# Kernel optimization log

Hardware: AMD Instinct MI355X
Metric: run time of the kernel (lower is better)

Reference implementation:

```python
import jax, jax.numpy as jnp
import numpy as np
import math

D, S, B = 64, 2048, 16  # head_dim, seq_len, batch (inputs stored as [D, S, B])


def setup_inputs() -> dict:
    key = jax.random.key(0)
    kq, kk, kv = jax.random.split(key, 3)
    return {
        "Q": jax.random.normal(kq, (D, S, B), dtype=jnp.float32),
        "K": jax.random.normal(kk, (D, S, B), dtype=jnp.float32),
        "V": jax.random.normal(kv, (D, S, B), dtype=jnp.float32),
        "d_k": S,
    }


def reference(Q, K, V, d_k):
    # transpose(0, 2): [D, S, B] -> [B, S, D]
    q = jnp.transpose(Q, (2, 1, 0))
    k = jnp.transpose(K, (2, 1, 0))
    v = jnp.transpose(V, (2, 1, 0))
    # bmm(_Q, K_T) * 1/sqrt(d_k): [B, S, S]
    scores = jnp.einsum("bsd,btd->bst", q, k) * (1.0 / math.sqrt(d_k))
    # original does view(-1, d_k) + Softmax over dim=1; with d_k == last dim
    # this is a softmax over the key axis. Dropout is identity in eval mode.
    probs = jax.nn.softmax(scores, axis=-1)
    out = jnp.einsum("bst,btd->bsd", probs, v)  # [B, S, D]
    # transpose(0, 2) back: [D, S, B]
    return jnp.transpose(out, (2, 1, 0))
```

## Files before the change

kernel.cpp:

```cpp
#include <hip/hip_runtime.h>

#define D_ 64
#define S_ 2048
#define B_ 16
#define QT 64
#define KVT 128

typedef short short8 __attribute__((ext_vector_type(8)));
typedef short short4a __attribute__((ext_vector_type(4)));
typedef float floatx4 __attribute__((ext_vector_type(4)));
typedef unsigned uint2v __attribute__((ext_vector_type(2)));

#define SC2 (1.4426950408889634f / 45.254833995939045f)

__device__ __forceinline__ unsigned short f2bf(float f) {
  unsigned u = __builtin_bit_cast(unsigned, f);
  u += 0x7fffu + ((u >> 16) & 1u);
  return (unsigned short)(u >> 16);
}

__device__ __forceinline__ floatx4 mfma16(short4a a, short4a b, floatx4 c) {
#if __has_builtin(__builtin_amdgcn_mfma_f32_16x16x16bf16_1k)
  return __builtin_amdgcn_mfma_f32_16x16x16bf16_1k(a, b, c, 0, 0, 0);
#else
  floatx4 d;
  asm volatile("v_mfma_f32_16x16x16_bf16 %0, %1, %2, %3"
               : "=v"(d) : "v"(a), "v"(b), "v"(c));
  return d;
#endif
}

__global__ __launch_bounds__(256) void pack_all(const float* __restrict__ Q,
                                                const float* __restrict__ K,
                                                const float* __restrict__ V,
                                                unsigned short* __restrict__ Qp,
                                                unsigned short* __restrict__ Kp,
                                                unsigned short* __restrict__ Vt) {
  __shared__ __align__(16) unsigned short tile[256][72];
  const int t = threadIdx.x;
  const int bid = blockIdx.x;
  if (bid < 256) {
    const bool isK = bid >= 128;
    const float* src = isK ? K : Q;
    unsigned short* dst = isK ? Kp : Qp;
    const float scale = isK ? SC2 : 1.0f;
    const int rb = bid & 127;
    const int s0 = rb * 16;
#pragma unroll
    for (int i = 0; i < 16; i++) {
      int j = i * 256 + t;
      int d = j >> 6;
      int sb4 = (j & 63) * 4;
      const float4 v = *(const float4*)(src + (size_t)d * (S_ * B_) + s0 * B_ + sb4);
      float vv[4] = {v.x, v.y, v.z, v.w};
#pragma unroll
      for (int k = 0; k < 4; k++) {
        int sb = sb4 + k;
        tile[(sb & 15) * 16 + (sb >> 4)][d] = f2bf(vv[k] * scale);
      }
    }
    __syncthreads();
#pragma unroll
    for (int i = 0; i < 8; i++) {
      int j = i * 256 + t;
      int r = j >> 3, c = j & 7;
      int b = r >> 4, si = r & 15;
      uint4 v = *(const uint4*)(&tile[r][c * 8]);
      *(uint4*)(dst + (((size_t)(b * 128 + rb)) << 10) + ((c >> 2) << 9) +
                (((c & 3) * 16 + si) << 3)) = v;
    }
  } else {
    const int vb = bid - 256;
    const int s0 = (vb & 31) * 64;
    const int d0 = (vb >> 5) * 16;
    const int dblk = vb >> 5;
#pragma unroll
    for (int i = 0; i < 16; i++) {
      int j = i * 256 + t;
      int dd = j >> 8;
      int sb4 = (j & 255) * 4;
      const float4 v = *(const float4*)(V + (size_t)(d0 + dd) * (S_ * B_) + s0 * B_ + sb4);
      float vv[4] = {v.x, v.y, v.z, v.w};
#pragma unroll
      for (int k = 0; k < 4; k++) {
        int sb = sb4 + k;
        tile[(sb & 15) * 16 + dd][sb >> 4] = f2bf(vv[k]);
      }
    }
    __syncthreads();
#pragma unroll
    for (int i = 0; i < 8; i++) {
      int j = i * 256 + t;
      int r = j >> 3, c = j & 7;
      int b = r >> 4, dd = r & 15;
      uint4 v = *(const uint4*)(&tile[r][c * 8]);
      int kvblk = (vb & 31) * 4 + (c >> 1);
      int g0 = (c & 1) * 2;
      size_t a0 = (((size_t)(b * 128 + kvblk) * 4 + dblk) << 8) + ((g0 * 16 + dd) << 2);
      *(uint2*)(Vt + a0) = make_uint2(v.x, v.y);
      *(uint2*)(Vt + a0 + 64) = make_uint2(v.z, v.w);
    }
  }
}

__global__ __launch_bounds__(256, 2) void attn(const unsigned short* __restrict__ Qp,
                                               const unsigned short* __restrict__ Kp,
                                               const unsigned short* __restrict__ Vt,
                                               float* __restrict__ Ot) {
  __shared__ __align__(16) char smem_[69632 + 1024];
  float* red = (float*)smem_;
  float* lred = (float*)(smem_ + 69632);

  const int tid = threadIdx.x;
  const int w = tid >> 6, l = tid & 63, g = l >> 4, ln = l & 15;
  const int b = blockIdx.x & 15;
  const int q0 = (int)(blockIdx.x >> 4) * QT;

  const unsigned short* Qb = Qp + ((size_t)b << 17);
  const unsigned short* Kb = Kp + ((size_t)b << 17);
  const unsigned short* Vb = Vt + ((size_t)b << 17);

  const unsigned short* Qw = Qb + (((size_t)(q0 >> 4)) << 10) + l * 8;
  const unsigned short* Kw = Kb + w * 2048 + l * 8;
  const unsigned short* Vw = Vb + w * 2048 + l * 4;

  short8 qf[4][2];
#pragma unroll
  for (int nf = 0; nf < 4; nf++)
#pragma unroll
    for (int ks = 0; ks < 2; ks++)
      qf[nf][ks] = *(const short8*)(Qw + nf * 1024 + ks * 512);

  short8 kf[2][2];
#pragma unroll
  for (int mf = 0; mf < 2; mf++)
#pragma unroll
    for (int ks = 0; ks < 2; ks++)
      kf[mf][ks] = *(const short8*)(Kw + mf * 1024 + ks * 512);

  short4a vf[4][2];
#pragma unroll
  for (int mfd = 0; mfd < 4; mfd++)
#pragma unroll
    for (int mf = 0; mf < 2; mf++)
      vf[mfd][mf] = *(const short4a*)(Vw + mf * 1024 + mfd * 256);

  const short4a ones = {(short)0x3F80, (short)0x3F80, (short)0x3F80, (short)0x3F80};
  floatx4 oacc[4][4];
  floatx4 dacc[4];
#pragma unroll
  for (int mfd = 0; mfd < 4; mfd++)
#pragma unroll
    for (int nf = 0; nf < 4; nf++) oacc[mfd][nf] = (floatx4){0.f, 0.f, 0.f, 0.f};
#pragma unroll
  for (int nf = 0; nf < 4; nf++) dacc[nf] = (floatx4){0.f, 0.f, 0.f, 0.f};

  for (int t = 0; t < 16; t++) {
    const int tn = (((t + 1) & 15)) * 8192;

    floatx4 sacc[2][4];
#pragma unroll
    for (int mf = 0; mf < 2; mf++)
#pragma unroll
      for (int nf = 0; nf < 4; nf++) sacc[mf][nf] = (floatx4){0.f, 0.f, 0.f, 0.f};
    __builtin_amdgcn_s_setprio(1);
#pragma unroll
    for (int ks = 0; ks < 2; ks++)
#pragma unroll
      for (int mf = 0; mf < 2; mf++)
#pragma unroll
        for (int nf = 0; nf < 4; nf++)
          sacc[mf][nf] = __builtin_amdgcn_mfma_f32_16x16x32_bf16(kf[mf][ks], qf[nf][ks],
                                                                 sacc[mf][nf], 0, 0, 0);
    __builtin_amdgcn_s_setprio(0);

#pragma unroll
    for (int mf = 0; mf < 2; mf++)
#pragma unroll
      for (int ks = 0; ks < 2; ks++)
        kf[mf][ks] = *(const short8*)(Kw + tn + mf * 1024 + ks * 512);

    short4a pb[2][4];
#pragma unroll
    for (int mf = 0; mf < 2; mf++)
#pragma unroll
      for (int nf = 0; nf < 4; nf++) {
        unsigned u0 = __builtin_bit_cast(unsigned, __builtin_amdgcn_exp2f(sacc[mf][nf][0])) + 0x8000u;
        unsigned u1 = __builtin_bit_cast(unsigned, __builtin_amdgcn_exp2f(sacc[mf][nf][1])) + 0x8000u;
        unsigned u2 = __builtin_bit_cast(unsigned, __builtin_amdgcn_exp2f(sacc[mf][nf][2])) + 0x8000u;
        unsigned u3 = __builtin_bit_cast(unsigned, __builtin_amdgcn_exp2f(sacc[mf][nf][3])) + 0x8000u;
        unsigned lo = __builtin_amdgcn_perm(u1, u0, 0x07060302u);
        unsigned hi = __builtin_amdgcn_perm(u3, u2, 0x07060302u);
        pb[mf][nf] = __builtin_bit_cast(short4a, (uint2v){lo, hi});
      }

    __builtin_amdgcn_s_setprio(1);
#pragma unroll
    for (int mf = 0; mf < 2; mf++)
#pragma unroll
      for (int nf = 0; nf < 4; nf++)
        dacc[nf] = mfma16(ones, pb[mf][nf], dacc[nf]);

#pragma unroll
    for (int mfd = 0; mfd < 4; mfd++)
#pragma unroll
      for (int mf = 0; mf < 2; mf++) {
#pragma unroll
        for (int nf = 0; nf < 4; nf++)
          oacc[mfd][nf] = mfma16(vf[mfd][mf], pb[mf][nf], oacc[mfd][nf]);
      }
    __builtin_amdgcn_s_setprio(0);

#pragma unroll
    for (int mfd = 0; mfd < 4; mfd++)
#pragma unroll
      for (int mf = 0; mf < 2; mf++)
        vf[mfd][mf] = *(const short4a*)(Vw + tn + mf * 1024 + mfd * 256);
  }

  if (g == 0) {
#pragma unroll
    for (int nf = 0; nf < 4; nf++) lred[w * 64 + nf * 16 + ln] = dacc[nf][0];
  }
#pragma unroll
  for (int mfd = 0; mfd < 4; mfd++)
#pragma unroll
    for (int nf = 0; nf < 4; nf++)
      *(floatx4*)(&red[w * 4352 + (nf * 16 + ln) * 68 + mfd * 16 + g * 4]) = oacc[mfd][nf];
  __syncthreads();

  const int q = l;
  const float denom = lred[q] + lred[64 + q] + lred[128 + q] + lred[192 + q];
  const float linv = 1.0f / denom;
#pragma unroll
  for (int i = 0; i < 4; i++) {
    floatx4 s = (floatx4){0.f, 0.f, 0.f, 0.f};
#pragma unroll
    for (int w2 = 0; w2 < 4; w2++)
      s += *(const floatx4*)(&red[w2 * 4352 + q * 68 + w * 16 + i * 4]);
    s *= linv;
#pragma unroll
    for (int r = 0; r < 4; r++)
      Ot[(size_t)(b * D_ + w * 16 + i * 4 + r) * S_ + q0 + q] = s[r];
  }
}

__global__ __launch_bounds__(256) void unpack_o(const float* __restrict__ Ot,
                                                float* __restrict__ out) {
  const int d0 = (int)(blockIdx.x & 7) * 8;
  const int s0 = (int)(blockIdx.x >> 3) * 64;
  __shared__ float u[8 * 1024];
  const int t = threadIdx.x;
#pragma unroll
  for (int i = 0; i < 8; i++) {
    int j = i * 256 + t;
    int d = j >> 8, bb = (j >> 4) & 15, c = j & 15;
    float4 v = *(const float4*)(Ot + (size_t)(bb * D_ + d0 + d) * S_ + s0 + c * 4);
    float vv[4] = {v.x, v.y, v.z, v.w};
#pragma unroll
    for (int k = 0; k < 4; k++) {
      int si = c * 4 + k;
      int W = si * 16 + bb;
      int Wp = W ^ ((si & 15) << 2);
      u[d * 1024 + Wp] = vv[k];
    }
  }
  __syncthreads();
#pragma unroll
  for (int i = 0; i < 8; i++) {
    int j = i * 256 + t;
    int d = j >> 8, c2 = j & 255;
    int G = c2 ^ ((c2 >> 2) & 15);
    float4 v = *(const float4*)(&u[d * 1024 + G * 4]);
    *(float4*)(out + (size_t)(d0 + d) * (S_ * B_) + s0 * B_ + c2 * 4) = v;
  }
}

extern "C" void kernel_launch(void* const* d_in, const int* in_sizes, int n_in,
                              void* d_out, int out_size, void* d_ws, size_t ws_size,
                              hipStream_t stream) {
  const float* Q = (const float*)d_in[0];
  const float* K = (const float*)d_in[1];
  const float* V = (const float*)d_in[2];
  float* out = (float*)d_out;
  char* ws = (char*)d_ws;
  unsigned short* Qp = (unsigned short*)(ws);
  unsigned short* Kp = (unsigned short*)(ws + (4u << 20));
  unsigned short* Vt = (unsigned short*)(ws + (8u << 20));
  float* Ot = (float*)(ws + (12u << 20));

  hipLaunchKernelGGL(pack_all, dim3(384), dim3(256), 0, stream, Q, K, V, Qp, Kp, Vt);
  hipLaunchKernelGGL(attn, dim3(512), dim3(256), 0, stream, Qp, Kp, Vt, Ot);
  hipLaunchKernelGGL(unpack_o, dim3(256), dim3(256), 0, stream, Ot, out);
}
```

Baseline: 104.3 us.

## Split attention over KV halves and merge partial sums in unpack

Splits the key/value sequence into two halves handled by separate blocks (split-K style), doubling the grid to 1024 blocks. Each block writes unnormalized partial outputs and denominators, and the unpack kernel sums both halves and applies the reciprocal denominator. Halving the reduction shared memory and raising launch bounds to 4 blocks per SM is meant to improve occupancy and fill more CUs on the mi355x. In exchange it adds extra global traffic for two partial output buffers plus an extra sync in the reduction. Combining the partials without per-half max rescaling matches the existing kernel, which also does not appear to track a running max.

```diff
diff --git a/kernel.cpp b/kernel.cpp
--- a/kernel.cpp
+++ b/kernel.cpp
@@ -103,26 +103,28 @@
   }
 }
 
-__global__ __launch_bounds__(256, 2) void attn(const unsigned short* __restrict__ Qp,
+__global__ __launch_bounds__(256, 4) void attn(const unsigned short* __restrict__ Qp,
                                                const unsigned short* __restrict__ Kp,
                                                const unsigned short* __restrict__ Vt,
-                                               float* __restrict__ Ot) {
-  __shared__ __align__(16) char smem_[69632 + 1024];
+                                               float* __restrict__ Otp,
+                                               float* __restrict__ Dp) {
+  __shared__ __align__(16) char smem_[34816 + 1024];
   float* red = (float*)smem_;
-  float* lred = (float*)(smem_ + 69632);
+  float* lred = (float*)(smem_ + 34816);
 
   const int tid = threadIdx.x;
   const int w = tid >> 6, l = tid & 63, g = l >> 4, ln = l & 15;
   const int b = blockIdx.x & 15;
-  const int q0 = (int)(blockIdx.x >> 4) * QT;
+  const int q0 = ((int)(blockIdx.x >> 4) & 31) * QT;
+  const int h = (int)(blockIdx.x >> 9);
 
   const unsigned short* Qb = Qp + ((size_t)b << 17);
   const unsigned short* Kb = Kp + ((size_t)b << 17);
   const unsigned short* Vb = Vt + ((size_t)b << 17);
 
   const unsigned short* Qw = Qb + (((size_t)(q0 >> 4)) << 10) + l * 8;
-  const unsigned short* Kw = Kb + w * 2048 + l * 8;
-  const unsigned short* Vw = Vb + w * 2048 + l * 4;
+  const unsigned short* Kw = Kb + h * 65536 + w * 2048 + l * 8;
+  const unsigned short* Vw = Vb + h * 65536 + w * 2048 + l * 4;
 
   short8 qf[4][2];
 #pragma unroll
@@ -155,8 +157,8 @@
 #pragma unroll
   for (int nf = 0; nf < 4; nf++) dacc[nf] = (floatx4){0.f, 0.f, 0.f, 0.f};
 
-  for (int t = 0; t < 16; t++) {
-    const int tn = (((t + 1) & 15)) * 8192;
+  for (int t = 0; t < 8; t++) {
+    const int tn = ((t + 1) & 7) * 8192;
 
     floatx4 sacc[2][4];
 #pragma unroll
@@ -222,47 +224,73 @@
 #pragma unroll
     for (int nf = 0; nf < 4; nf++) lred[w * 64 + nf * 16 + ln] = dacc[nf][0];
   }
-#pragma unroll
-  for (int mfd = 0; mfd < 4; mfd++)
-#pragma unroll
-    for (int nf = 0; nf < 4; nf++)
-      *(floatx4*)(&red[w * 4352 + (nf * 16 + ln) * 68 + mfd * 16 + g * 4]) = oacc[mfd][nf];
+  if (w < 2) {
+#pragma unroll
+    for (int mfd = 0; mfd < 4; mfd++)
+#pragma unroll
+      for (int nf = 0; nf < 4; nf++)
+        *(floatx4*)(&red[w * 4352 + (nf * 16 + ln) * 68 + mfd * 16 + g * 4]) = oacc[mfd][nf];
+  }
   __syncthreads();
+  if (w >= 2) {
+#pragma unroll
+    for (int mfd = 0; mfd < 4; mfd++)
+#pragma unroll
+      for (int nf = 0; nf < 4; nf++) {
+        float* p = &red[(w - 2) * 4352 + (nf * 16 + ln) * 68 + mfd * 16 + g * 4];
+        *(floatx4*)p = *(const floatx4*)p + oacc[mfd][nf];
+      }
+  }
+  __syncthreads();
 
   const int q = l;
-  const float denom = lred[q] + lred[64 + q] + lred[128 + q] + lred[192 + q];
-  const float linv = 1.0f / denom;
+  if (w == 0) {
+    const float denom = lred[q] + lred[64 + q] + lred[128 + q] + lred[192 + q];
+    Dp[(size_t)h * (B_ * S_) + (size_t)b * S_ + q0 + q] = denom;
+  }
+  float* Oth = Otp + (size_t)h * ((size_t)B_ * D_ * S_);
 #pragma unroll
   for (int i = 0; i < 4; i++) {
-    floatx4 s = (floatx4){0.f, 0.f, 0.f, 0.f};
-#pragma unroll
-    for (int w2 = 0; w2 < 4; w2++)
-      s += *(const floatx4*)(&red[w2 * 4352 + q * 68 + w * 16 + i * 4]);
-    s *= linv;
+    floatx4 s = *(const floatx4*)(&red[q * 68 + w * 16 + i * 4]) +
+                *(const floatx4*)(&red[4352 + q * 68 + w * 16 + i * 4]);
 #pragma unroll
     for (int r = 0; r < 4; r++)
-      Ot[(size_t)(b * D_ + w * 16 + i * 4 + r) * S_ + q0 + q] = s[r];
-  }
-}
-
-__global__ __launch_bounds__(256) void unpack_o(const float* __restrict__ Ot,
+      Oth[(size_t)(b * D_ + w * 16 + i * 4 + r) * S_ + q0 + q] = s[r];
+  }
+}
+
+__global__ __launch_bounds__(256) void unpack_o(const float* __restrict__ Ot0,
+                                                const float* __restrict__ Ot1,
+                                                const float* __restrict__ Dp0,
+                                                const float* __restrict__ Dp1,
                                                 float* __restrict__ out) {
   const int d0 = (int)(blockIdx.x & 7) * 8;
   const int s0 = (int)(blockIdx.x >> 3) * 64;
   __shared__ float u[8 * 1024];
+  __shared__ float linv_s[1024];
   const int t = threadIdx.x;
+#pragma unroll
+  for (int k = 0; k < 4; k++) {
+    int idx = k * 256 + t;
+    int bb = idx >> 6, si = idx & 63;
+    float dsum = Dp0[(size_t)bb * S_ + s0 + si] + Dp1[(size_t)bb * S_ + s0 + si];
+    linv_s[idx] = 1.0f / dsum;
+  }
+  __syncthreads();
 #pragma unroll
   for (int i = 0; i < 8; i++) {
     int j = i * 256 + t;
     int d = j >> 8, bb = (j >> 4) & 15, c = j & 15;
-    float4 v = *(const float4*)(Ot + (size_t)(bb * D_ + d0 + d) * S_ + s0 + c * 4);
-    float vv[4] = {v.x, v.y, v.z, v.w};
+    const size_t off = (size_t)(bb * D_ + d0 + d) * S_ + s0 + c * 4;
+    float4 v0 = *(const float4*)(Ot0 + off);
+    float4 v1 = *(const float4*)(Ot1 + off);
+    float vv[4] = {v0.x + v1.x, v0.y + v1.y, v0.z + v1.z, v0.w + v1.w};
 #pragma unroll
     for (int k = 0; k < 4; k++) {
       int si = c * 4 + k;
       int W = si * 16 + bb;
       int Wp = W ^ ((si & 15) << 2);
-      u[d * 1024 + Wp] = vv[k];
+      u[d * 1024 + Wp] = vv[k] * linv_s[bb * 64 + si];
     }
   }
   __syncthreads();
@@ -287,9 +315,11 @@
   unsigned short* Qp = (unsigned short*)(ws);
   unsigned short* Kp = (unsigned short*)(ws + (4u << 20));
   unsigned short* Vt = (unsigned short*)(ws + (8u << 20));
-  float* Ot = (float*)(ws + (12u << 20));
+  float* Otp = (float*)(ws + (12u << 20));
+  float* Dp = (float*)(ws + (28u << 20));
 
   hipLaunchKernelGGL(pack_all, dim3(384), dim3(256), 0, stream, Q, K, V, Qp, Kp, Vt);
-  hipLaunchKernelGGL(attn, dim3(512), dim3(256), 0, stream, Qp, Kp, Vt, Ot);
-  hipLaunchKernelGGL(unpack_o, dim3(256), dim3(256), 0, stream, Ot, out);
-}
+  hipLaunchKernelGGL(attn, dim3(1024), dim3(256), 0, stream, Qp, Kp, Vt, Otp, Dp);
+  hipLaunchKernelGGL(unpack_o, dim3(256), dim3(256), 0, stream,
+                     Otp, Otp + (size_t)B_ * D_ * S_, Dp, Dp + (size_t)B_ * S_, out);
+}
```

Result: slower. 215.1 us (+106.2%).

## Use 16x16x32 bf16 MFMA for PV and denominator with repacked V layout

Applied to the files above, without the earlier changes.

Replaces the pairs of 16x16x16 MFMAs in the P·V and row-sum steps with single 16x16x32 bf16 MFMAs. Two P fragments are concatenated into one short8 per query fragment, and the V pack kernel is rewritten so each lane loads one contiguous 16-byte short8 per output fragment. This halves the MFMA instruction count in the second GEMM and widens the V loads. In exchange, the K-chunk layout of P and V must match exactly in both kernels, which adds a correctness risk.

```diff
diff --git a/kernel.cpp b/kernel.cpp
--- a/kernel.cpp
+++ b/kernel.cpp
@@ -10,6 +10,7 @@
 typedef short short4a __attribute__((ext_vector_type(4)));
 typedef float floatx4 __attribute__((ext_vector_type(4)));
 typedef unsigned uint2v __attribute__((ext_vector_type(2)));
+typedef unsigned uint4v __attribute__((ext_vector_type(4)));
 
 #define SC2 (1.4426950408889634f / 45.254833995939045f)
 
@@ -17,17 +18,6 @@
   unsigned u = __builtin_bit_cast(unsigned, f);
   u += 0x7fffu + ((u >> 16) & 1u);
   return (unsigned short)(u >> 16);
-}
-
-__device__ __forceinline__ floatx4 mfma16(short4a a, short4a b, floatx4 c) {
-#if __has_builtin(__builtin_amdgcn_mfma_f32_16x16x16bf16_1k)
-  return __builtin_amdgcn_mfma_f32_16x16x16bf16_1k(a, b, c, 0, 0, 0);
-#else
-  floatx4 d;
-  asm volatile("v_mfma_f32_16x16x16_bf16 %0, %1, %2, %3"
-               : "=v"(d) : "v"(a), "v"(b), "v"(c));
-  return d;
-#endif
 }
 
 __global__ __launch_bounds__(256) void pack_all(const float* __restrict__ Q,
@@ -91,14 +81,15 @@
 #pragma unroll
     for (int i = 0; i < 8; i++) {
       int j = i * 256 + t;
-      int r = j >> 3, c = j & 7;
-      int b = r >> 4, dd = r & 15;
-      uint4 v = *(const uint4*)(&tile[r][c * 8]);
-      int kvblk = (vb & 31) * 4 + (c >> 1);
-      int g0 = (c & 1) * 2;
-      size_t a0 = (((size_t)(b * 128 + kvblk) * 4 + dblk) << 8) + ((g0 * 16 + dd) << 2);
-      *(uint2*)(Vt + a0) = make_uint2(v.x, v.y);
-      *(uint2*)(Vt + a0 + 64) = make_uint2(v.z, v.w);
+      int b = j >> 7;
+      int c32r = (j >> 6) & 1;
+      int l = j & 63, g = l >> 4, ln = l & 15;
+      const unsigned short* row = &tile[b * 16 + ln][c32r * 32];
+      uint2 u0 = *(const uint2*)(row + g * 4);
+      uint2 u1 = *(const uint2*)(row + 16 + g * 4);
+      int c32 = (s0 >> 5) + c32r;
+      uint4 o = make_uint4(u0.x, u0.y, u1.x, u1.y);
+      *(uint4*)(Vt + (((size_t)(b * 64 + c32) * 4 + dblk) << 9) + l * 8) = o;
     }
   }
 }
@@ -122,7 +113,7 @@
 
   const unsigned short* Qw = Qb + (((size_t)(q0 >> 4)) << 10) + l * 8;
   const unsigned short* Kw = Kb + w * 2048 + l * 8;
-  const unsigned short* Vw = Vb + w * 2048 + l * 4;
+  const unsigned short* Vw = Vb + w * 2048 + l * 8;
 
   short8 qf[4][2];
 #pragma unroll
@@ -138,14 +129,13 @@
     for (int ks = 0; ks < 2; ks++)
       kf[mf][ks] = *(const short8*)(Kw + mf * 1024 + ks * 512);
 
-  short4a vf[4][2];
+  short8 vf[4];
 #pragma unroll
   for (int mfd = 0; mfd < 4; mfd++)
-#pragma unroll
-    for (int mf = 0; mf < 2; mf++)
-      vf[mfd][mf] = *(const short4a*)(Vw + mf * 1024 + mfd * 256);
-
-  const short4a ones = {(short)0x3F80, (short)0x3F80, (short)0x3F80, (short)0x3F80};
+    vf[mfd] = *(const short8*)(Vw + mfd * 512);
+
+  const short8 ones8 = {(short)0x3F80, (short)0x3F80, (short)0x3F80, (short)0x3F80,
+                        (short)0x3F80, (short)0x3F80, (short)0x3F80, (short)0x3F80};
   floatx4 oacc[4][4];
   floatx4 dacc[4];
 #pragma unroll
@@ -156,7 +146,7 @@
   for (int nf = 0; nf < 4; nf++) dacc[nf] = (floatx4){0.f, 0.f, 0.f, 0.f};
 
   for (int t = 0; t < 16; t++) {
-    const int tn = (((t + 1) & 15)) * 8192;
+    const int tn = ((t + 1) & 15) * 8192;
 
     floatx4 sacc[2][4];
 #pragma unroll
@@ -180,42 +170,39 @@
       for (int ks = 0; ks < 2; ks++)
         kf[mf][ks] = *(const short8*)(Kw + tn + mf * 1024 + ks * 512);
 
-    short4a pb[2][4];
-#pragma unroll
-    for (int mf = 0; mf < 2; mf++)
-#pragma unroll
-      for (int nf = 0; nf < 4; nf++) {
+    short8 pbf[4];
+#pragma unroll
+    for (int nf = 0; nf < 4; nf++) {
+      uint2v pu[2];
+#pragma unroll
+      for (int mf = 0; mf < 2; mf++) {
         unsigned u0 = __builtin_bit_cast(unsigned, __builtin_amdgcn_exp2f(sacc[mf][nf][0])) + 0x8000u;
         unsigned u1 = __builtin_bit_cast(unsigned, __builtin_amdgcn_exp2f(sacc[mf][nf][1])) + 0x8000u;
         unsigned u2 = __builtin_bit_cast(unsigned, __builtin_amdgcn_exp2f(sacc[mf][nf][2])) + 0x8000u;
         unsigned u3 = __builtin_bit_cast(unsigned, __builtin_amdgcn_exp2f(sacc[mf][nf][3])) + 0x8000u;
         unsigned lo = __builtin_amdgcn_perm(u1, u0, 0x07060302u);
         unsigned hi = __builtin_amdgcn_perm(u3, u2, 0x07060302u);
-        pb[mf][nf] = __builtin_bit_cast(short4a, (uint2v){lo, hi});
+        pu[mf] = (uint2v){lo, hi};
       }
+      pbf[nf] = __builtin_bit_cast(short8, (uint4v){pu[0][0], pu[0][1], pu[1][0], pu[1][1]});
+    }
 
     __builtin_amdgcn_s_setprio(1);
 #pragma unroll
-    for (int mf = 0; mf < 2; mf++)
+    for (int nf = 0; nf < 4; nf++)
+      dacc[nf] = __builtin_amdgcn_mfma_f32_16x16x32_bf16(ones8, pbf[nf], dacc[nf], 0, 0, 0);
+
+#pragma unroll
+    for (int mfd = 0; mfd < 4; mfd++)
 #pragma unroll
       for (int nf = 0; nf < 4; nf++)
-        dacc[nf] = mfma16(ones, pb[mf][nf], dacc[nf]);
+        oacc[mfd][nf] = __builtin_amdgcn_mfma_f32_16x16x32_bf16(vf[mfd], pbf[nf],
+                                                                oacc[mfd][nf], 0, 0, 0);
+    __builtin_amdgcn_s_setprio(0);
 
 #pragma unroll
     for (int mfd = 0; mfd < 4; mfd++)
-#pragma unroll
-      for (int mf = 0; mf < 2; mf++) {
-#pragma unroll
-        for (int nf = 0; nf < 4; nf++)
-          oacc[mfd][nf] = mfma16(vf[mfd][mf], pb[mf][nf], oacc[mfd][nf]);
-      }
-    __builtin_amdgcn_s_setprio(0);
-
-#pragma unroll
-    for (int mfd = 0; mfd < 4; mfd++)
-#pragma unroll
-      for (int mf = 0; mf < 2; mf++)
-        vf[mfd][mf] = *(const short4a*)(Vw + tn + mf * 1024 + mfd * 256);
+      vf[mfd] = *(const short8*)(Vw + tn + mfd * 512);
   }
 
   if (g == 0) {
```

New measurement: 100.0 us. 4.1% less time.
